# Kernel tuning notes

Measured on AMD Instinct MI355X. Metric: run time of the kernel, lower is better.

The kernel has to match this reference:

```python
import jax, jax.numpy as jnp
import numpy as np

N, D, F_NUM = 262144, 128, 64
TEMPERATURE = 0.5
EPS = 1e-8  # torch F.cosine_similarity eps


def setup_inputs() -> dict:
    key = jax.random.key(0)
    k1, k2 = jax.random.split(key)
    embeddings = jax.random.normal(k1, (N, D), dtype=jnp.float32)
    families = jax.random.randint(k2, (N,), 0, F_NUM, dtype=jnp.int32)
    return {"embeddings": embeddings, "families": families}


def reference(embeddings, families):
    T = TEMPERATURE
    n = embeddings.shape[0]
    # Per-family prototype means (segment mean). All F_NUM families are
    # present w.h.p.; guard counts with max(.,1) to avoid div-by-zero.
    ones = jnp.ones((n,), dtype=embeddings.dtype)
    counts = jax.ops.segment_sum(ones, families, num_segments=F_NUM)
    sums = jax.ops.segment_sum(embeddings, families, num_segments=F_NUM)
    protos = sums / jnp.maximum(counts, 1.0)[:, None]  # [F, D]

    # Cosine similarity matrix [N, F], matching torch eps semantics:
    # x.y / max(||x|| * ||y||, eps)
    dots = embeddings @ protos.T                              # [N, F]
    e_norm = jnp.linalg.norm(embeddings, axis=1)              # [N]
    p_norm = jnp.linalg.norm(protos, axis=1)                  # [F]
    sim = dots / jnp.maximum(e_norm[:, None] * p_norm[None, :], EPS)

    pos = jnp.take_along_axis(sim, families[:, None].astype(jnp.int32), axis=1)[:, 0]  # [N]
    # Source quirk: logits already divided by T, then divided by T again
    # inside logsumexp -> effective sim / T^2. The concatenated logits
    # contain pos + all other prototypes = all F prototypes exactly once.
    lse = jax.nn.logsumexp(sim / (T * T), axis=1)             # [N]
    per_sample = -pos / T + lse                               # [N]
    loss = jnp.sum(per_sample) / n
    return loss[None]  # torch returns shape (1,)
```

## Files before the change

### kernel.cpp

```cpp
#include <hip/hip_runtime.h>
#include <math.h>


#define D_DIM 128
#define F_NUM 64

typedef __attribute__((ext_vector_type(8))) short short8;
typedef __attribute__((ext_vector_type(4))) float f32x4;

static __device__ __forceinline__ unsigned short f2bf(float x) {
  union { float f; unsigned u; } v; v.f = x;
  unsigned r = v.u + 0x7FFFu + ((v.u >> 16) & 1u);
  return (unsigned short)(r >> 16);
}

__global__ __launch_bounds__(256) void pass_a(
    const float* __restrict__ emb, const int* __restrict__ fam,
    float* __restrict__ psum, unsigned int* __restrict__ ehat)
{
  __shared__ float acc[4 * F_NUM * D_DIM];
  int t = threadIdx.x;
  float4 z = make_float4(0.f, 0.f, 0.f, 0.f);
  float4* a4 = (float4*)acc;
  #pragma unroll
  for (int k = 0; k < 32; ++k) a4[t + k * 256] = z;
  __syncthreads();

  int w = t >> 6, l = t & 63;
  float* my = acc + w * 8192;
  int base = __builtin_amdgcn_readfirstlane(blockIdx.x * 1024 + w * 256);
  const float2* e2 = (const float2*)emb;

  #pragma unroll 1
  for (int b = 0; b < 16; ++b) {
    float2 v[16]; int f[16];
    #pragma unroll
    for (int j = 0; j < 16; ++j) {
      int r = base + b * 16 + j;
      v[j] = e2[(size_t)r * 64 + l];
      f[j] = fam[r];
    }
    #pragma unroll
    for (int j = 0; j < 16; ++j) {
      float x = v[j].x, y = v[j].y;
      float nq = x * x + y * y;
      nq += __shfl_xor(nq, 1);  nq += __shfl_xor(nq, 2);  nq += __shfl_xor(nq, 4);
      nq += __shfl_xor(nq, 8);  nq += __shfl_xor(nq, 16); nq += __shfl_xor(nq, 32);
      float inv = rsqrtf(fmaxf(nq, 1e-20f));
      ehat[(size_t)(base + b * 16 + j) * 64 + l] =
          ((unsigned)f2bf(y * inv) << 16) | f2bf(x * inv);
      float2* dst = (float2*)&my[f[j] * D_DIM + 2 * l];
      float2 cur = *dst;
      cur.x += x; cur.y += y;
      *dst = cur;
    }
  }
  __syncthreads();

  float4* out4 = (float4*)(psum + (size_t)blockIdx.x * (F_NUM * D_DIM));
  #pragma unroll
  for (int k = 0; k < 8; ++k) {
    int idx4 = t + k * 256;
    float4 r = z;
    #pragma unroll
    for (int rp = 0; rp < 4; ++rp) {
      float4 a = a4[rp * 2048 + idx4];
      r.x += a.x; r.y += a.y; r.z += a.z; r.w += a.w;
    }
    out4[idx4] = r;
  }
}

__global__ __launch_bounds__(256) void pass_b1(
    const float* __restrict__ psum, float* __restrict__ protoRaw, int nPart)
{
  __shared__ float red[256];
  int f = blockIdx.x >> 2, qd = blockIdx.x & 3;
  int t = threadIdx.x;
  int d = qd * 32 + (t & 31), p0 = t >> 5;
  int per = nPart >> 3;
  float s = 0.f;
  #pragma unroll 8
  for (int i = 0; i < per; ++i)
    s += psum[(size_t)(p0 + 8 * i) * (F_NUM * D_DIM) + f * D_DIM + d];
  red[t] = s;
  __syncthreads();
  if (t < 32) {
    float r = 0.f;
    #pragma unroll
    for (int k = 0; k < 8; ++k) r += red[k * 32 + t];
    protoRaw[f * D_DIM + qd * 32 + t] = r;
  }
}

__global__ __launch_bounds__(256) void pass_b2(
    const float* __restrict__ protoRaw, unsigned short* __restrict__ protoB)
{
  int t = threadIdx.x, f = t >> 2, pt = t & 3;
  const float4* src = (const float4*)(protoRaw + f * D_DIM + pt * 32);
  float4 v[8];
  float n2 = 0.f;
  #pragma unroll
  for (int i = 0; i < 8; ++i) {
    v[i] = src[i];
    n2 += v[i].x * v[i].x + v[i].y * v[i].y + v[i].z * v[i].z + v[i].w * v[i].w;
  }
  n2 += __shfl_xor(n2, 1);
  n2 += __shfl_xor(n2, 2);
  float inv = rsqrtf(fmaxf(n2, 1e-24f));
  ushort4* dst = (ushort4*)(protoB + f * D_DIM + pt * 32);
  #pragma unroll
  for (int i = 0; i < 8; ++i) {
    ushort4 u;
    u.x = f2bf(v[i].x * inv); u.y = f2bf(v[i].y * inv);
    u.z = f2bf(v[i].z * inv); u.w = f2bf(v[i].w * inv);
    dst[i] = u;
  }
}

__global__ __launch_bounds__(256) void pass_c(
    const unsigned short* __restrict__ ehat, const int* __restrict__ fam,
    const unsigned short* __restrict__ protoB,
    float* __restrict__ out, float invN)
{
  __shared__ __align__(16) unsigned short sA[128 * 136];
  __shared__ __align__(16) unsigned short sB[F_NUM * 136];
  __shared__ int   sFam[128];
  __shared__ float sWp[4];

  int t = threadIdx.x;
  int R0 = blockIdx.x * 128;
  const short8* srcA = (const short8*)ehat;
  const short8* srcB = (const short8*)protoB;

  #pragma unroll
  for (int it = 0; it < 8; ++it) {
    int idx = it * 256 + t;
    int row = idx >> 4, c8 = idx & 15;
    *(short8*)&sA[row * 136 + c8 * 8] = srcA[(size_t)(R0 + row) * 16 + c8];
  }
  #pragma unroll
  for (int it = 0; it < 4; ++it) {
    int idx = it * 256 + t;
    int row = idx >> 4, c8 = idx & 15;
    *(short8*)&sB[row * 136 + c8 * 8] = srcB[idx];
  }
  if (t < 128) sFam[t] = fam[R0 + t];
  __syncthreads();

  int w = t >> 6, lane = t & 63, m16 = lane & 15, q = lane >> 4;

  f32x4 acc[2][4] = {};
  const unsigned short* aB0 = &sA[(w * 32 + m16) * 136 + q * 8];
  const unsigned short* aB1 = aB0 + 16 * 136;
  const unsigned short* bB  = &sB[m16 * 136 + q * 8];

  #pragma unroll
  for (int ks = 0; ks < 4; ++ks) {
    int ko = ks * 32;
    short8 a0 = *(const short8*)(aB0 + ko);
    short8 a1 = *(const short8*)(aB1 + ko);
    short8 b0 = *(const short8*)(bB + ko);
    short8 b1 = *(const short8*)(bB + 16 * 136 + ko);
    short8 b2 = *(const short8*)(bB + 32 * 136 + ko);
    short8 b3 = *(const short8*)(bB + 48 * 136 + ko);
    acc[0][0] = __builtin_amdgcn_mfma_f32_16x16x32_bf16(a0, b0, acc[0][0], 0, 0, 0);
    acc[0][1] = __builtin_amdgcn_mfma_f32_16x16x32_bf16(a0, b1, acc[0][1], 0, 0, 0);
    acc[0][2] = __builtin_amdgcn_mfma_f32_16x16x32_bf16(a0, b2, acc[0][2], 0, 0, 0);
    acc[0][3] = __builtin_amdgcn_mfma_f32_16x16x32_bf16(a0, b3, acc[0][3], 0, 0, 0);
    acc[1][0] = __builtin_amdgcn_mfma_f32_16x16x32_bf16(a1, b0, acc[1][0], 0, 0, 0);
    acc[1][1] = __builtin_amdgcn_mfma_f32_16x16x32_bf16(a1, b1, acc[1][1], 0, 0, 0);
    acc[1][2] = __builtin_amdgcn_mfma_f32_16x16x32_bf16(a1, b2, acc[1][2], 0, 0, 0);
    acc[1][3] = __builtin_amdgcn_mfma_f32_16x16x32_bf16(a1, b3, acc[1][3], 0, 0, 0);
  }

  float wp = 0.f;
  #pragma unroll
  for (int rt = 0; rt < 2; ++rt) {
    #pragma unroll
    for (int i = 0; i < 4; ++i) {
      int row = w * 32 + rt * 16 + q * 4 + i;
      int fr = sFam[row], frh = fr >> 4, frl = fr & 15;
      float es = 0.f, ps = 0.f;
      #pragma unroll
      for (int ft = 0; ft < 4; ++ft) {
        float sim = acc[rt][ft][i];
        es += __expf(4.f * sim - 4.f);
        if (frl == m16 && frh == ft) ps = sim;
      }
      #pragma unroll
      for (int off = 1; off < 16; off <<= 1) {
        es += __shfl_xor(es, off);
        ps += __shfl_xor(ps, off);
      }
      if (m16 == 0) wp += 4.f + __logf(es) - 2.f * ps;
    }
  }
  wp += __shfl_xor(wp, 16);
  wp += __shfl_xor(wp, 32);
  if (lane == 0) sWp[w] = wp;
  __syncthreads();
  if (t == 0)
    unsafeAtomicAdd(out, (sWp[0] + sWp[1] + sWp[2] + sWp[3]) * invN);
}

extern "C" void kernel_launch(void* const* d_in, const int* in_sizes, int n_in,
                              void* d_out, int out_size, void* d_ws, size_t ws_size,
                              hipStream_t stream) {
  const float* emb = (const float*)d_in[0];
  const int* fam = (const int*)d_in[1];
  int N = in_sizes[0] / D_DIM;
  int blocksA = N / 1024;
  int blocksC = N / 128;

  float* ws = (float*)d_ws;
  float* psum = ws;
  size_t off = (size_t)blocksA * (F_NUM * D_DIM);
  float* protoRaw = ws + off;                off += F_NUM * D_DIM;
  unsigned short* protoB = (unsigned short*)(ws + off); off += (F_NUM * D_DIM) / 2;
  unsigned int* ehat = (unsigned int*)(ws + off);

  (void)hipMemsetAsync(d_out, 0, sizeof(float), stream);
  pass_a<<<blocksA, 256, 0, stream>>>(emb, fam, psum, ehat);
  pass_b1<<<4 * F_NUM, 256, 0, stream>>>(psum, protoRaw, blocksA);
  pass_b2<<<1, 256, 0, stream>>>(protoRaw, protoB);
  pass_c<<<blocksC, 256, 0, stream>>>((const unsigned short*)ehat, fam, protoB,
                                      (float*)d_out, 1.0f / (float)N);
}
```

Baseline: 250.4 us.

## Use 1024-thread pass_a with LDS atomics, direct-load pass_c, fold memset

pass_a now runs 1024-thread blocks in which 16 waves share 4 LDS accumulators. Each wave updates them with atomicAdd, and the per-row loads are split into two coalesced float halves instead of float2. The ehat layout changes to interleave the lo/hi halves, and pass_b2 permutes the prototype bf16 layout to match. pass_c drops its LDS staging and loads A and B fragments and family ids straight from global memory into registers. The output memset is folded into pass_b2. The risks are LDS atomic contention and lower occupancy in pass_a, and uncached repeated global fragment loads in pass_c.

```diff
diff --git a/kernel.cpp b/kernel.cpp
--- a/kernel.cpp
+++ b/kernel.cpp
@@ -14,7 +14,7 @@
   return (unsigned short)(r >> 16);
 }
 
-__global__ __launch_bounds__(256) void pass_a(
+__global__ __launch_bounds__(1024) void pass_a(
     const float* __restrict__ emb, const int* __restrict__ fam,
     float* __restrict__ psum, unsigned int* __restrict__ ehat)
 {
@@ -23,44 +23,41 @@
   float4 z = make_float4(0.f, 0.f, 0.f, 0.f);
   float4* a4 = (float4*)acc;
   #pragma unroll
-  for (int k = 0; k < 32; ++k) a4[t + k * 256] = z;
+  for (int k = 0; k < 8; ++k) a4[t + k * 1024] = z;
   __syncthreads();
 
   int w = t >> 6, l = t & 63;
-  float* my = acc + w * 8192;
-  int base = __builtin_amdgcn_readfirstlane(blockIdx.x * 1024 + w * 256);
-  const float2* e2 = (const float2*)emb;
+  float* my = acc + (w & 3) * (F_NUM * D_DIM);
+  int base = __builtin_amdgcn_readfirstlane(blockIdx.x * 1024 + w * 64);
 
   #pragma unroll 1
-  for (int b = 0; b < 16; ++b) {
-    float2 v[16]; int f[16];
+  for (int b = 0; b < 4; ++b) {
+    float x[16], y[16]; int f[16];
     #pragma unroll
     for (int j = 0; j < 16; ++j) {
       int r = base + b * 16 + j;
-      v[j] = e2[(size_t)r * 64 + l];
+      x[j] = emb[(size_t)r * D_DIM + l];
+      y[j] = emb[(size_t)r * D_DIM + 64 + l];
       f[j] = fam[r];
     }
     #pragma unroll
     for (int j = 0; j < 16; ++j) {
-      float x = v[j].x, y = v[j].y;
-      float nq = x * x + y * y;
+      float nq = x[j] * x[j] + y[j] * y[j];
       nq += __shfl_xor(nq, 1);  nq += __shfl_xor(nq, 2);  nq += __shfl_xor(nq, 4);
       nq += __shfl_xor(nq, 8);  nq += __shfl_xor(nq, 16); nq += __shfl_xor(nq, 32);
       float inv = rsqrtf(fmaxf(nq, 1e-20f));
       ehat[(size_t)(base + b * 16 + j) * 64 + l] =
-          ((unsigned)f2bf(y * inv) << 16) | f2bf(x * inv);
-      float2* dst = (float2*)&my[f[j] * D_DIM + 2 * l];
-      float2 cur = *dst;
-      cur.x += x; cur.y += y;
-      *dst = cur;
+          ((unsigned)f2bf(y[j] * inv) << 16) | f2bf(x[j] * inv);
+      atomicAdd(&my[f[j] * D_DIM + l], x[j]);
+      atomicAdd(&my[f[j] * D_DIM + 64 + l], y[j]);
     }
   }
   __syncthreads();
 
   float4* out4 = (float4*)(psum + (size_t)blockIdx.x * (F_NUM * D_DIM));
   #pragma unroll
-  for (int k = 0; k < 8; ++k) {
-    int idx4 = t + k * 256;
+  for (int k = 0; k < 2; ++k) {
+    int idx4 = t + k * 1024;
     float4 r = z;
     #pragma unroll
     for (int rp = 0; rp < 4; ++rp) {
@@ -94,16 +91,22 @@
 }
 
 __global__ __launch_bounds__(256) void pass_b2(
-    const float* __restrict__ protoRaw, unsigned short* __restrict__ protoB)
+    const float* __restrict__ protoRaw, unsigned short* __restrict__ protoB,
+    float* __restrict__ out)
 {
   int t = threadIdx.x, f = t >> 2, pt = t & 3;
-  const float4* src = (const float4*)(protoRaw + f * D_DIM + pt * 32);
-  float4 v[8];
+  if (t == 0) out[0] = 0.f;
+  const float4* lo4 = (const float4*)(protoRaw + f * D_DIM + pt * 16);
+  const float4* hi4 = (const float4*)(protoRaw + f * D_DIM + 64 + pt * 16);
+  float lo[16], hi[16];
   float n2 = 0.f;
   #pragma unroll
-  for (int i = 0; i < 8; ++i) {
-    v[i] = src[i];
-    n2 += v[i].x * v[i].x + v[i].y * v[i].y + v[i].z * v[i].z + v[i].w * v[i].w;
+  for (int i = 0; i < 4; ++i) {
+    float4 a = lo4[i], b = hi4[i];
+    lo[4 * i + 0] = a.x; lo[4 * i + 1] = a.y; lo[4 * i + 2] = a.z; lo[4 * i + 3] = a.w;
+    hi[4 * i + 0] = b.x; hi[4 * i + 1] = b.y; hi[4 * i + 2] = b.z; hi[4 * i + 3] = b.w;
+    n2 += a.x * a.x + a.y * a.y + a.z * a.z + a.w * a.w;
+    n2 += b.x * b.x + b.y * b.y + b.z * b.z + b.w * b.w;
   }
   n2 += __shfl_xor(n2, 1);
   n2 += __shfl_xor(n2, 2);
@@ -112,8 +115,8 @@
   #pragma unroll
   for (int i = 0; i < 8; ++i) {
     ushort4 u;
-    u.x = f2bf(v[i].x * inv); u.y = f2bf(v[i].y * inv);
-    u.z = f2bf(v[i].z * inv); u.w = f2bf(v[i].w * inv);
+    u.x = f2bf(lo[2 * i] * inv);     u.y = f2bf(hi[2 * i] * inv);
+    u.z = f2bf(lo[2 * i + 1] * inv); u.w = f2bf(hi[2 * i + 1] * inv);
     dst[i] = u;
   }
 }
@@ -123,55 +126,42 @@
     const unsigned short* __restrict__ protoB,
     float* __restrict__ out, float invN)
 {
-  __shared__ __align__(16) unsigned short sA[128 * 136];
-  __shared__ __align__(16) unsigned short sB[F_NUM * 136];
-  __shared__ int   sFam[128];
   __shared__ float sWp[4];
-
   int t = threadIdx.x;
   int R0 = blockIdx.x * 128;
-  const short8* srcA = (const short8*)ehat;
-  const short8* srcB = (const short8*)protoB;
-
-  #pragma unroll
-  for (int it = 0; it < 8; ++it) {
-    int idx = it * 256 + t;
-    int row = idx >> 4, c8 = idx & 15;
-    *(short8*)&sA[row * 136 + c8 * 8] = srcA[(size_t)(R0 + row) * 16 + c8];
-  }
-  #pragma unroll
-  for (int it = 0; it < 4; ++it) {
-    int idx = it * 256 + t;
-    int row = idx >> 4, c8 = idx & 15;
-    *(short8*)&sB[row * 136 + c8 * 8] = srcB[idx];
-  }
-  if (t < 128) sFam[t] = fam[R0 + t];
-  __syncthreads();
-
   int w = t >> 6, lane = t & 63, m16 = lane & 15, q = lane >> 4;
 
+  const short8* A16 = (const short8*)ehat;
+  const short8* B16 = (const short8*)protoB;
+
+  int frv[2][4];
+  #pragma unroll
+  for (int rt = 0; rt < 2; ++rt)
+    #pragma unroll
+    for (int i = 0; i < 4; ++i)
+      frv[rt][i] = fam[R0 + w * 32 + rt * 16 + q * 4 + i];
+
+  short8 bfr[4][4];
+  #pragma unroll
+  for (int ks = 0; ks < 4; ++ks)
+    #pragma unroll
+    for (int ft = 0; ft < 4; ++ft)
+      bfr[ks][ft] = B16[(ft * 16 + m16) * 16 + ks * 4 + q];
+
+  size_t aBase = (size_t)(R0 + w * 32 + m16) * 16 + q;
   f32x4 acc[2][4] = {};
-  const unsigned short* aB0 = &sA[(w * 32 + m16) * 136 + q * 8];
-  const unsigned short* aB1 = aB0 + 16 * 136;
-  const unsigned short* bB  = &sB[m16 * 136 + q * 8];
-
   #pragma unroll
   for (int ks = 0; ks < 4; ++ks) {
-    int ko = ks * 32;
-    short8 a0 = *(const short8*)(aB0 + ko);
-    short8 a1 = *(const short8*)(aB1 + ko);
-    short8 b0 = *(const short8*)(bB + ko);
-    short8 b1 = *(const short8*)(bB + 16 * 136 + ko);
-    short8 b2 = *(const short8*)(bB + 32 * 136 + ko);
-    short8 b3 = *(const short8*)(bB + 48 * 136 + ko);
-    acc[0][0] = __builtin_amdgcn_mfma_f32_16x16x32_bf16(a0, b0, acc[0][0], 0, 0, 0);
-    acc[0][1] = __builtin_amdgcn_mfma_f32_16x16x32_bf16(a0, b1, acc[0][1], 0, 0, 0);
-    acc[0][2] = __builtin_amdgcn_mfma_f32_16x16x32_bf16(a0, b2, acc[0][2], 0, 0, 0);
-    acc[0][3] = __builtin_amdgcn_mfma_f32_16x16x32_bf16(a0, b3, acc[0][3], 0, 0, 0);
-    acc[1][0] = __builtin_amdgcn_mfma_f32_16x16x32_bf16(a1, b0, acc[1][0], 0, 0, 0);
-    acc[1][1] = __builtin_amdgcn_mfma_f32_16x16x32_bf16(a1, b1, acc[1][1], 0, 0, 0);
-    acc[1][2] = __builtin_amdgcn_mfma_f32_16x16x32_bf16(a1, b2, acc[1][2], 0, 0, 0);
-    acc[1][3] = __builtin_amdgcn_mfma_f32_16x16x32_bf16(a1, b3, acc[1][3], 0, 0, 0);
+    short8 a0 = A16[aBase + ks * 4];
+    short8 a1 = A16[aBase + 256 + ks * 4];
+    acc[0][0] = __builtin_amdgcn_mfma_f32_16x16x32_bf16(a0, bfr[ks][0], acc[0][0], 0, 0, 0);
+    acc[0][1] = __builtin_amdgcn_mfma_f32_16x16x32_bf16(a0, bfr[ks][1], acc[0][1], 0, 0, 0);
+    acc[0][2] = __builtin_amdgcn_mfma_f32_16x16x32_bf16(a0, bfr[ks][2], acc[0][2], 0, 0, 0);
+    acc[0][3] = __builtin_amdgcn_mfma_f32_16x16x32_bf16(a0, bfr[ks][3], acc[0][3], 0, 0, 0);
+    acc[1][0] = __builtin_amdgcn_mfma_f32_16x16x32_bf16(a1, bfr[ks][0], acc[1][0], 0, 0, 0);
+    acc[1][1] = __builtin_amdgcn_mfma_f32_16x16x32_bf16(a1, bfr[ks][1], acc[1][1], 0, 0, 0);
+    acc[1][2] = __builtin_amdgcn_mfma_f32_16x16x32_bf16(a1, bfr[ks][2], acc[1][2], 0, 0, 0);
+    acc[1][3] = __builtin_amdgcn_mfma_f32_16x16x32_bf16(a1, bfr[ks][3], acc[1][3], 0, 0, 0);
   }
 
   float wp = 0.f;
@@ -179,8 +169,7 @@
   for (int rt = 0; rt < 2; ++rt) {
     #pragma unroll
     for (int i = 0; i < 4; ++i) {
-      int row = w * 32 + rt * 16 + q * 4 + i;
-      int fr = sFam[row], frh = fr >> 4, frl = fr & 15;
+      int fr = frv[rt][i], frh = fr >> 4, frl = fr & 15;
       float es = 0.f, ps = 0.f;
       #pragma unroll
       for (int ft = 0; ft < 4; ++ft) {
@@ -220,10 +209,9 @@
   unsigned short* protoB = (unsigned short*)(ws + off); off += (F_NUM * D_DIM) / 2;
   unsigned int* ehat = (unsigned int*)(ws + off);
 
-  (void)hipMemsetAsync(d_out, 0, sizeof(float), stream);
-  pass_a<<<blocksA, 256, 0, stream>>>(emb, fam, psum, ehat);
+  pass_a<<<blocksA, 1024, 0, stream>>>(emb, fam, psum, ehat);
   pass_b1<<<4 * F_NUM, 256, 0, stream>>>(psum, protoRaw, blocksA);
-  pass_b2<<<1, 256, 0, stream>>>(protoRaw, protoB);
+  pass_b2<<<1, 256, 0, stream>>>(protoRaw, protoB, (float*)d_out);
   pass_c<<<blocksC, 256, 0, stream>>>((const unsigned short*)ehat, fam, protoB,
                                       (float*)d_out, 1.0f / (float)N);
 }
```

After: 373.5 us. +49.2%, slower.
